# Optimization experiments

Measured on AMD Instinct MI355X. Metric: run time of the kernel, lower is better.

Reference implementation:

```python
import jax, jax.numpy as jnp
import numpy as np

B, L, D = 8192, 200, 64
NUM_ITEMS = 100000
HID = 64  # attention hidden_dim


def setup_inputs() -> dict:
    key = jax.random.key(0)
    ks = jax.random.split(key, 16)
    inp = {
        "item_sequence": jax.random.randint(ks[0], (B, L), 0, NUM_ITEMS),
        "click_sequence": jax.random.randint(ks[1], (B, L), 0, 2),
        "seq_length": jax.random.randint(ks[2], (B, 1), 1, L + 1),
        "target_item": jax.random.randint(ks[3], (B, 1), 0, NUM_ITEMS),
        "context_features": jax.random.normal(ks[4], (B, 9), dtype=jnp.float32),
        # embedding table (num_items+1, D)
        "emb_table": jax.random.normal(ks[5], (NUM_ITEMS + 1, D), dtype=jnp.float32) * 0.05,
        # attention MLP: Linear(2D->64), Linear(64->32), Linear(32->1)
        "aw1": jax.random.normal(ks[6], (2 * D, HID), dtype=jnp.float32) * 0.05,
        "ab1": jnp.zeros((HID,), jnp.float32),
        "aw2": jax.random.normal(ks[7], (HID, HID // 2), dtype=jnp.float32) * 0.05,
        "ab2": jnp.zeros((HID // 2,), jnp.float32),
        "aw3": jax.random.normal(ks[8], (HID // 2, 1), dtype=jnp.float32) * 0.05,
        "ab3": jnp.zeros((1,), jnp.float32),
        # context MLP: Linear(9->32)
        "cw": jax.random.normal(ks[9], (9, 32), dtype=jnp.float32) * 0.05,
        "cb": jnp.zeros((32,), jnp.float32),
        # head MLP: Linear(160->128), Linear(128->64), Linear(64->1)
        "mw1": jax.random.normal(ks[10], (2 * D + 32, 128), dtype=jnp.float32) * 0.05,
        "mb1": jnp.zeros((128,), jnp.float32),
        "mw2": jax.random.normal(ks[11], (128, 64), dtype=jnp.float32) * 0.05,
        "mb2": jnp.zeros((64,), jnp.float32),
        "mw3": jax.random.normal(ks[12], (64, 1), dtype=jnp.float32) * 0.05,
        "mb3": jnp.zeros((1,), jnp.float32),
    }
    return inp


def reference(item_sequence, click_sequence, seq_length, target_item, context_features,
              emb_table, aw1, ab1, aw2, ab2, aw3, ab3, cw, cb,
              mw1, mb1, mw2, mb2, mw3, mb3):
    seq_emb = emb_table[item_sequence]                 # [B, L, D]
    tgt_emb = emb_table[target_item[:, 0]]             # [B, D]
    seq_len = item_sequence.shape[1]
    mask = (jnp.arange(seq_len)[None, :] < seq_length).astype(seq_emb.dtype)  # [B, L]

    # DIN attention: concat(query, keys) -> 3-layer MLP -> masked softmax -> weighted sum
    q = jnp.broadcast_to(tgt_emb[:, None, :], seq_emb.shape)          # [B, L, D]
    att_in = jnp.concatenate([q, seq_emb], axis=-1)                   # [B, L, 2D]
    h = jax.nn.relu(att_in @ aw1 + ab1)
    h = jax.nn.relu(h @ aw2 + ab2)
    scores = (h @ aw3 + ab3)[..., 0]                                  # [B, L]
    scores = jnp.where(mask == 0, jnp.asarray(-1e9, scores.dtype), scores)
    w = jax.nn.softmax(scores, axis=1)                                # [B, L]
    attended = jnp.einsum('bl,bld->bd', w, seq_emb)                   # [B, D]

    ctx = jax.nn.relu(context_features @ cw + cb)                     # [B, 32]
    comb = jnp.concatenate([attended, tgt_emb, ctx], axis=1)          # [B, 2D+32]
    h = jax.nn.relu(comb @ mw1 + mb1)
    h = jax.nn.relu(h @ mw2 + mb2)
    out = jax.nn.sigmoid(h @ mw3 + mb3)[:, 0]                         # [B]
    return out
```

## Files before the change

kernel.cpp:

```cpp
#include <hip/hip_runtime.h>
#include <cmath>

typedef __attribute__((ext_vector_type(8))) short s16x8;
typedef __attribute__((ext_vector_type(4))) short s16x4;
typedef __attribute__((ext_vector_type(4))) float f32x4;

__device__ __forceinline__ short f2bf(float f) {
    union { float f; unsigned u; } v; v.f = f;
    unsigned r = v.u + 0x7FFFu + ((v.u >> 16) & 1u);
    return (short)(r >> 16);
}
__device__ __forceinline__ float bf2f(short s) {
    union { unsigned u; float f; } v; v.u = ((unsigned)(unsigned short)s) << 16;
    return v.f;
}

#define EMB_ELEMS 6400064
#define W1SEQ_SH  6400064
#define W1TOP_SH  6404160
#define W2_SH     6408256
#define MW1T_SH   6410304
#define MW2T_SH   6430784
#define QC_F      3219488
#define SC_F      3743776
#define CB_SH     10764352


__global__ __launch_bounds__(256)
void din_prep_kernel(const float* __restrict__ emb,
                     const float* __restrict__ aw1,
                     const float* __restrict__ aw2,
                     const float* __restrict__ mw1,
                     const float* __restrict__ mw2,
                     short* __restrict__ ws)
{
    const int bid = blockIdx.x;
    const int t = threadIdx.x;
    if (bid < 6251) {
        long e4 = ((long)bid * 256 + t) * 4;
        if (e4 < EMB_ELEMS) {
            float4 v = *(const float4*)(emb + e4);
            s16x4 bv = { f2bf(v.x), f2bf(v.y), f2bf(v.z), f2bf(v.w) };
            *(s16x4*)(ws + e4) = bv;
        }
        return;
    }
    const int wb = bid - 6251;
    if (wb == 0) {
        for (int idx = t; idx < 4096; idx += 256) {
            int j = idx & 7, lane = (idx >> 3) & 63, fr = idx >> 9;
            int n = (fr >> 1) * 16 + (lane & 15);
            int k = (fr & 1) * 32 + (lane >> 4) * 8 + j;
            ws[W1SEQ_SH + idx] = f2bf(aw1[(64 + k) * 64 + n]);
        }
    } else if (wb == 1) {
        for (int idx = t; idx < 4096; idx += 256) {
            int j = idx & 7, lane = (idx >> 3) & 63, fr = idx >> 9;
            int n = (fr >> 1) * 16 + (lane & 15);
            int k = (fr & 1) * 32 + (lane >> 4) * 8 + j;
            ws[W1TOP_SH + idx] = f2bf(aw1[k * 64 + n]);
        }
    } else if (wb == 2) {
        for (int idx = t; idx < 2048; idx += 256) {
            int j = idx & 7, lane = (idx >> 3) & 63, fr = idx >> 9;
            int n = (fr >> 1) * 16 + (lane & 15);
            int k = (fr & 1) * 32 + (lane >> 4) * 8 + j;
            ws[W2_SH + idx] = f2bf(aw2[k * 32 + n]);
        }
    } else if (wb == 3) {
        for (int idx = t; idx < 8192; idx += 256) {
            int j = idx & 7, lane = (idx >> 3) & 63, fr = idx >> 9;
            int n = (fr >> 2) * 16 + (lane & 15);
            int k = (fr & 3) * 32 + (lane >> 4) * 8 + j;
            ws[MW2T_SH + idx] = f2bf(mw2[k * 64 + n]);
        }
    } else {
        const int base = (wb - 4) * 5120;
        for (int ii = t; ii < 5120; ii += 256) {
            int idx = base + ii;
            int j = idx & 7, lane = (idx >> 3) & 63, fr = idx >> 9;
            int nt = fr / 5, ks = fr - nt * 5;
            int n = nt * 16 + (lane & 15);
            int k = ks * 32 + (lane >> 4) * 8 + j;
            ws[MW1T_SH + idx] = f2bf(mw1[k * 128 + n]);
        }
    }
}

__global__ __launch_bounds__(256)
void din_qc_kernel(const int* __restrict__ tgt_item,
                   const float* __restrict__ ab1,
                   short* __restrict__ ws)
{
    const int t = threadIdx.x, lane = t & 63, wave = t >> 6;
    const int quad = lane >> 4, r16 = lane & 15;
    const short* embbf = ws;
    const short* w1t   = ws + W1TOP_SH;
    float* qc = (float*)ws + QC_F;

    const int b0 = (blockIdx.x * 4 + wave) * 16;
    const int it = tgt_item[b0 + r16];
    const short* rp = embbf + it * 64 + quad * 8;
    s16x8 a0 = *(const s16x8*)(rp);
    s16x8 a1 = *(const s16x8*)(rp + 32);

    f32x4 acc[4] = {{0,0,0,0},{0,0,0,0},{0,0,0,0},{0,0,0,0}};
    #pragma unroll
    for (int nt = 0; nt < 4; ++nt) {
        s16x8 b_0 = *(const s16x8*)(w1t + ((nt * 2 + 0) * 64 + lane) * 8);
        s16x8 b_1 = *(const s16x8*)(w1t + ((nt * 2 + 1) * 64 + lane) * 8);
        acc[nt] = __builtin_amdgcn_mfma_f32_16x16x32_bf16(a0, b_0, acc[nt], 0, 0, 0);
        acc[nt] = __builtin_amdgcn_mfma_f32_16x16x32_bf16(a1, b_1, acc[nt], 0, 0, 0);
    }
    #pragma unroll
    for (int nt = 0; nt < 4; ++nt) {
        float bias = ab1[nt * 16 + r16];
        #pragma unroll
        for (int rr = 0; rr < 4; ++rr)
            qc[(b0 + quad * 4 + rr) * 64 + nt * 16 + r16] = acc[nt][rr] + bias;
    }
}

#define H1_PITCH 72
__global__ __launch_bounds__(256)
void din_att_kernel(const int* __restrict__ item_seq,
                    const int* __restrict__ seq_len_p,
                    const float* __restrict__ ab2,
                    const float* __restrict__ aw3, const float* __restrict__ ab3,
                    short* __restrict__ ws)
{
    const int t = threadIdx.x, lane = t & 63, wave = t >> 6;
    const int quad = lane >> 4, r16 = lane & 15;
    __shared__ short s_w1[4096];
    __shared__ short s_h1[4][16 * H1_PITCH];

    {
        const s16x8* src = (const s16x8*)(ws + W1SEQ_SH);
        s16x8* dst = (s16x8*)s_w1;
        for (int i = t; i < 512; i += 256) dst[i] = src[i];
    }
    __syncthreads();

    const int b    = blockIdx.x;
    const int len  = seq_len_p[b];
    const int row0 = wave * 64;
    if (row0 >= len) return;
    const int nc = min(4, (len - row0 + 15) >> 4);

    const short* embbf = ws;
    const float* qc    = (const float*)ws + QC_F + b * 64;
    float* scores      = (float*)ws + SC_F + b * 200;

    s16x8 af[4][2];
    #pragma unroll
    for (int ck = 0; ck < 4; ++ck) {
        if (ck < nc) {
            int r = row0 + ck * 16 + r16; if (r > 199) r = 199;
            const int it = item_seq[b * 200 + r];
            af[ck][0] = *(const s16x8*)(embbf + it * 64 + quad * 8);
            af[ck][1] = *(const s16x8*)(embbf + it * 64 + 32 + quad * 8);
        }
    }
    s16x8 w2r[4];
    #pragma unroll
    for (int fr = 0; fr < 4; ++fr)
        w2r[fr] = *(const s16x8*)(ws + W2_SH + (fr * 64 + lane) * 8);

    float qcv[4];
    #pragma unroll
    for (int nt = 0; nt < 4; ++nt) qcv[nt] = qc[nt * 16 + r16];
    const float bias2_lo = ab2[r16], bias2_hi = ab2[16 + r16];
    const float w3_lo    = aw3[r16], w3_hi    = aw3[16 + r16];
    const float b3       = ab3[0];
    short* h1w = s_h1[wave];

    #pragma unroll
    for (int ck = 0; ck < 4; ++ck) {
        if (ck >= nc) break;
        f32x4 acc[4] = {{0,0,0,0},{0,0,0,0},{0,0,0,0},{0,0,0,0}};
        #pragma unroll
        for (int nt = 0; nt < 4; ++nt) {
            s16x8 b_0 = *(const s16x8*)&s_w1[((nt * 2 + 0) * 64 + lane) * 8];
            s16x8 b_1 = *(const s16x8*)&s_w1[((nt * 2 + 1) * 64 + lane) * 8];
            acc[nt] = __builtin_amdgcn_mfma_f32_16x16x32_bf16(af[ck][0], b_0, acc[nt], 0, 0, 0);
            acc[nt] = __builtin_amdgcn_mfma_f32_16x16x32_bf16(af[ck][1], b_1, acc[nt], 0, 0, 0);
        }
        #pragma unroll
        for (int nt = 0; nt < 4; ++nt)
            #pragma unroll
            for (int rr = 0; rr < 4; ++rr) {
                float v = fmaxf(acc[nt][rr] + qcv[nt], 0.f);
                h1w[(quad * 4 + rr) * H1_PITCH + nt * 16 + r16] = f2bf(v);
            }
        __builtin_amdgcn_wave_barrier();

        s16x8 h0  = *(const s16x8*)&h1w[r16 * H1_PITCH + quad * 8];
        s16x8 h1v = *(const s16x8*)&h1w[r16 * H1_PITCH + 32 + quad * 8];
        f32x4 c2[2] = {{0,0,0,0},{0,0,0,0}};
        #pragma unroll
        for (int nt = 0; nt < 2; ++nt) {
            c2[nt] = __builtin_amdgcn_mfma_f32_16x16x32_bf16(h0,  w2r[nt * 2],     c2[nt], 0, 0, 0);
            c2[nt] = __builtin_amdgcn_mfma_f32_16x16x32_bf16(h1v, w2r[nt * 2 + 1], c2[nt], 0, 0, 0);
        }
        #pragma unroll
        for (int rr = 0; rr < 4; ++rr) {
            float p = fmaxf(c2[0][rr] + bias2_lo, 0.f) * w3_lo
                    + fmaxf(c2[1][rr] + bias2_hi, 0.f) * w3_hi;
            p += __shfl_xor(p, 8);
            p += __shfl_xor(p, 4);
            p += __shfl_xor(p, 2);
            p += __shfl_xor(p, 1);
            int orow = row0 + ck * 16 + quad * 4 + rr;
            if (r16 == 0 && orow < 200) scores[orow] = p + b3;
        }
        __builtin_amdgcn_wave_barrier();
    }
}

__global__ __launch_bounds__(256)
void din_pool_kernel(const int* __restrict__ item_seq,
                     const int* __restrict__ seq_len_p,
                     const int* __restrict__ tgt_item,
                     const float* __restrict__ ctx_feat,
                     const float* __restrict__ cw,  const float* __restrict__ cb,
                     short* __restrict__ ws)
{
    const int t = threadIdx.x, lane = t & 63, wave = t >> 6;
    const int quad = lane >> 4, r16 = lane & 15;
    __shared__ float s_w[4][200];

    const int b   = blockIdx.x * 4 + wave;
    const int len = seq_len_p[b];
    const short* embbf = ws;
    const float* sc    = (const float*)ws + SC_F + b * 200;
    short* comb        = ws + CB_SH + b * 160;

    float m = -1e30f;
    for (int l = lane; l < len; l += 64) m = fmaxf(m, sc[l]);
    #pragma unroll
    for (int off = 32; off; off >>= 1) m = fmaxf(m, __shfl_xor(m, off));
    float e = 0.f;
    for (int l = lane; l < len; l += 64) {
        float v = __expf(sc[l] - m);
        s_w[wave][l] = v;
        e += v;
    }
    #pragma unroll
    for (int off = 32; off; off >>= 1) e += __shfl_xor(e, off);
    const float inv = 1.f / e;
    __builtin_amdgcn_wave_barrier();

    float a0 = 0.f, a1 = 0.f, a2 = 0.f, a3 = 0.f;
    for (int l = quad; l < len; l += 8) {
        const int it0 = item_seq[b * 200 + l];
        s16x4 v0 = *(const s16x4*)(embbf + it0 * 64 + r16 * 4);
        const int l1 = l + 4;
        const bool live1 = l1 < len;
        s16x4 v1 = {};
        if (live1) {
            const int it1 = item_seq[b * 200 + l1];
            v1 = *(const s16x4*)(embbf + it1 * 64 + r16 * 4);
        }
        const float w0 = s_w[wave][l];
        const float w1 = live1 ? s_w[wave][l1] : 0.f;
        a0 += w0 * bf2f(v0.x) + w1 * bf2f(v1.x);
        a1 += w0 * bf2f(v0.y) + w1 * bf2f(v1.y);
        a2 += w0 * bf2f(v0.z) + w1 * bf2f(v1.z);
        a3 += w0 * bf2f(v0.w) + w1 * bf2f(v1.w);
    }
    a0 += __shfl_xor(a0, 16); a0 += __shfl_xor(a0, 32);
    a1 += __shfl_xor(a1, 16); a1 += __shfl_xor(a1, 32);
    a2 += __shfl_xor(a2, 16); a2 += __shfl_xor(a2, 32);
    a3 += __shfl_xor(a3, 16); a3 += __shfl_xor(a3, 32);
    if (quad == 0) {
        s16x4 bv = { f2bf(a0 * inv), f2bf(a1 * inv), f2bf(a2 * inv), f2bf(a3 * inv) };
        *(s16x4*)(comb + r16 * 4) = bv;
    }
    comb[64 + lane] = embbf[tgt_item[b] * 64 + lane];
    if (lane < 32) {
        float a = cb[lane];
        #pragma unroll
        for (int k = 0; k < 9; ++k) a += ctx_feat[b * 9 + k] * cw[k * 32 + lane];
        comb[128 + lane] = f2bf(fmaxf(a, 0.f));
    }
}

__global__ __launch_bounds__(256)
void din_mlp_kernel(const float* __restrict__ mb1,
                    const float* __restrict__ mb2,
                    const float* __restrict__ mw3, const float* __restrict__ mb3,
                    const short* __restrict__ ws,
                    float* __restrict__ out)
{
    const int t = threadIdx.x, lane = t & 63, wave = t >> 6;
    const int quad = lane >> 4, r16 = lane & 15;
    __shared__ short s_h1[4][16 * 136];
    __shared__ short s_h2[4][16 * 72];

    const int b0 = (blockIdx.x * 4 + wave) * 16;
    const short* comb = ws + CB_SH;
    const short* w1   = ws + MW1T_SH;
    const short* w2   = ws + MW2T_SH;

    s16x8 a[5];
    #pragma unroll
    for (int ks = 0; ks < 5; ++ks)
        a[ks] = *(const s16x8*)(comb + (b0 + r16) * 160 + ks * 32 + quad * 8);
    f32x4 acc[8] = {{0,0,0,0},{0,0,0,0},{0,0,0,0},{0,0,0,0},{0,0,0,0},{0,0,0,0},{0,0,0,0},{0,0,0,0}};
    #pragma unroll
    for (int nt = 0; nt < 8; ++nt)
        #pragma unroll
        for (int ks = 0; ks < 5; ++ks) {
            s16x8 bf = *(const s16x8*)(w1 + ((nt * 5 + ks) * 64 + lane) * 8);
            acc[nt] = __builtin_amdgcn_mfma_f32_16x16x32_bf16(a[ks], bf, acc[nt], 0, 0, 0);
        }
    #pragma unroll
    for (int nt = 0; nt < 8; ++nt) {
        float bias = mb1[nt * 16 + r16];
        #pragma unroll
        for (int rr = 0; rr < 4; ++rr)
            s_h1[wave][(quad * 4 + rr) * 136 + nt * 16 + r16] = f2bf(fmaxf(acc[nt][rr] + bias, 0.f));
    }
    __builtin_amdgcn_wave_barrier();

    s16x8 a2[4];
    #pragma unroll
    for (int ks = 0; ks < 4; ++ks)
        a2[ks] = *(const s16x8*)&s_h1[wave][r16 * 136 + ks * 32 + quad * 8];
    f32x4 acc2[4] = {{0,0,0,0},{0,0,0,0},{0,0,0,0},{0,0,0,0}};
    #pragma unroll
    for (int nt = 0; nt < 4; ++nt)
        #pragma unroll
        for (int ks = 0; ks < 4; ++ks) {
            s16x8 bf = *(const s16x8*)(w2 + ((nt * 4 + ks) * 64 + lane) * 8);
            acc2[nt] = __builtin_amdgcn_mfma_f32_16x16x32_bf16(a2[ks], bf, acc2[nt], 0, 0, 0);
        }
    #pragma unroll
    for (int nt = 0; nt < 4; ++nt) {
        float bias = mb2[nt * 16 + r16];
        #pragma unroll
        for (int rr = 0; rr < 4; ++rr)
            s_h2[wave][(quad * 4 + rr) * 72 + nt * 16 + r16] = f2bf(fmaxf(acc2[nt][rr] + bias, 0.f));
    }
    __builtin_amdgcn_wave_barrier();

    float p = 0.f;
    #pragma unroll
    for (int j = 0; j < 16; ++j)
        p += bf2f(s_h2[wave][r16 * 72 + quad * 16 + j]) * mw3[quad * 16 + j];
    p += __shfl_xor(p, 16);
    p += __shfl_xor(p, 32);
    if (quad == 0) out[b0 + r16] = 1.f / (1.f + __expf(-(p + mb3[0])));
}

extern "C" void kernel_launch(void* const* d_in, const int* in_sizes, int n_in,
                              void* d_out, int out_size, void* d_ws, size_t ws_size,
                              hipStream_t stream)
{
    const int*   item_seq  = (const int*)  d_in[0];
    const int*   seq_len   = (const int*)  d_in[2];
    const int*   tgt_item  = (const int*)  d_in[3];
    const float* ctx_feat  = (const float*)d_in[4];
    const float* emb       = (const float*)d_in[5];
    const float* aw1 = (const float*)d_in[6];
    const float* ab1 = (const float*)d_in[7];
    const float* aw2 = (const float*)d_in[8];
    const float* ab2 = (const float*)d_in[9];
    const float* aw3 = (const float*)d_in[10];
    const float* ab3 = (const float*)d_in[11];
    const float* cw  = (const float*)d_in[12];
    const float* cb  = (const float*)d_in[13];
    const float* mw1 = (const float*)d_in[14];
    const float* mb1 = (const float*)d_in[15];
    const float* mw2 = (const float*)d_in[16];
    const float* mb2 = (const float*)d_in[17];
    const float* mw3 = (const float*)d_in[18];
    const float* mb3 = (const float*)d_in[19];
    float* out = (float*)d_out;
    short* ws  = (short*)d_ws;

    hipLaunchKernelGGL(din_prep_kernel, dim3(6259), dim3(256), 0, stream,
                       emb, aw1, aw2, mw1, mw2, ws);
    hipLaunchKernelGGL(din_qc_kernel, dim3(128), dim3(256), 0, stream,
                       tgt_item, ab1, ws);
    hipLaunchKernelGGL(din_att_kernel, dim3(8192), dim3(256), 0, stream,
                       item_seq, seq_len, ab2, aw3, ab3, ws);
    hipLaunchKernelGGL(din_pool_kernel, dim3(2048), dim3(256), 0, stream,
                       item_seq, seq_len, tgt_item, ctx_feat, cw, cb, ws);
    hipLaunchKernelGGL(din_mlp_kernel, dim3(128), dim3(256), 0, stream,
                       mb1, mb2, mw3, mb3, ws, out);
}
```

Before: 197.8 us.

## Fuse query projection, attention scoring, softmax and pooling into one per-batch kernel

Folds the target-query projection, attention MLP scoring, masked softmax, weighted pooling and the context MLP into a single kernel with one block per batch row. Scores stay in shared memory, and the pooling reuses the embedding fragments already held in registers instead of gathering them from global memory a second time. This removes two kernel launches, the global round trip for scores and qc, and the duplicate embedding gather. The head MLP kernel is also reshaped into one wave per block with more blocks. In exchange, every block now does a mostly wasted MFMA for the single query row and pays extra block-wide syncs.

```diff
diff --git a/kernel.cpp b/kernel.cpp
--- a/kernel.cpp
+++ b/kernel.cpp
@@ -21,10 +21,7 @@
 #define W2_SH     6408256
 #define MW1T_SH   6410304
 #define MW2T_SH   6430784
-#define QC_F      3219488
-#define SC_F      3743776
 #define CB_SH     10764352
-
 
 __global__ __launch_bounds__(256)
 void din_prep_kernel(const float* __restrict__ emb,
@@ -87,70 +84,42 @@
     }
 }
 
-__global__ __launch_bounds__(256)
-void din_qc_kernel(const int* __restrict__ tgt_item,
-                   const float* __restrict__ ab1,
-                   short* __restrict__ ws)
-{
-    const int t = threadIdx.x, lane = t & 63, wave = t >> 6;
-    const int quad = lane >> 4, r16 = lane & 15;
-    const short* embbf = ws;
-    const short* w1t   = ws + W1TOP_SH;
-    float* qc = (float*)ws + QC_F;
-
-    const int b0 = (blockIdx.x * 4 + wave) * 16;
-    const int it = tgt_item[b0 + r16];
-    const short* rp = embbf + it * 64 + quad * 8;
-    s16x8 a0 = *(const s16x8*)(rp);
-    s16x8 a1 = *(const s16x8*)(rp + 32);
-
-    f32x4 acc[4] = {{0,0,0,0},{0,0,0,0},{0,0,0,0},{0,0,0,0}};
-    #pragma unroll
-    for (int nt = 0; nt < 4; ++nt) {
-        s16x8 b_0 = *(const s16x8*)(w1t + ((nt * 2 + 0) * 64 + lane) * 8);
-        s16x8 b_1 = *(const s16x8*)(w1t + ((nt * 2 + 1) * 64 + lane) * 8);
-        acc[nt] = __builtin_amdgcn_mfma_f32_16x16x32_bf16(a0, b_0, acc[nt], 0, 0, 0);
-        acc[nt] = __builtin_amdgcn_mfma_f32_16x16x32_bf16(a1, b_1, acc[nt], 0, 0, 0);
-    }
-    #pragma unroll
-    for (int nt = 0; nt < 4; ++nt) {
-        float bias = ab1[nt * 16 + r16];
-        #pragma unroll
-        for (int rr = 0; rr < 4; ++rr)
-            qc[(b0 + quad * 4 + rr) * 64 + nt * 16 + r16] = acc[nt][rr] + bias;
-    }
-}
-
 #define H1_PITCH 72
 __global__ __launch_bounds__(256)
-void din_att_kernel(const int* __restrict__ item_seq,
-                    const int* __restrict__ seq_len_p,
-                    const float* __restrict__ ab2,
-                    const float* __restrict__ aw3, const float* __restrict__ ab3,
-                    short* __restrict__ ws)
+void din_att_fused(const int* __restrict__ item_seq,
+                   const int* __restrict__ seq_len_p,
+                   const int* __restrict__ tgt_item,
+                   const float* __restrict__ ctx_feat,
+                   const float* __restrict__ ab1,
+                   const float* __restrict__ ab2,
+                   const float* __restrict__ aw3, const float* __restrict__ ab3,
+                   const float* __restrict__ cw,  const float* __restrict__ cb,
+                   short* __restrict__ ws)
 {
     const int t = threadIdx.x, lane = t & 63, wave = t >> 6;
     const int quad = lane >> 4, r16 = lane & 15;
     __shared__ short s_w1[4096];
     __shared__ short s_h1[4][16 * H1_PITCH];
+    __shared__ float s_sc[208];
+    __shared__ float s_qc[64];
+    __shared__ float s_pool[4][64];
+    __shared__ float s_ctx[32];
+    __shared__ float s_inv;
+
+    const int b   = blockIdx.x;
+    const int len = seq_len_p[b];
+    const int tgt = tgt_item[b];
+    const short* embbf = ws;
 
     {
         const s16x8* src = (const s16x8*)(ws + W1SEQ_SH);
         s16x8* dst = (s16x8*)s_w1;
-        for (int i = t; i < 512; i += 256) dst[i] = src[i];
-    }
-    __syncthreads();
-
-    const int b    = blockIdx.x;
-    const int len  = seq_len_p[b];
+        dst[t]       = src[t];
+        dst[t + 256] = src[t + 256];
+    }
+
     const int row0 = wave * 64;
-    if (row0 >= len) return;
-    const int nc = min(4, (len - row0 + 15) >> 4);
-
-    const short* embbf = ws;
-    const float* qc    = (const float*)ws + QC_F + b * 64;
-    float* scores      = (float*)ws + SC_F + b * 200;
-
+    const int nc = (row0 < len) ? min(4, (len - row0 + 15) >> 4) : 0;
     s16x8 af[4][2];
     #pragma unroll
     for (int ck = 0; ck < 4; ++ck) {
@@ -165,13 +134,35 @@
     #pragma unroll
     for (int fr = 0; fr < 4; ++fr)
         w2r[fr] = *(const s16x8*)(ws + W2_SH + (fr * 64 + lane) * 8);
-
-    float qcv[4];
-    #pragma unroll
-    for (int nt = 0; nt < 4; ++nt) qcv[nt] = qc[nt * 16 + r16];
     const float bias2_lo = ab2[r16], bias2_hi = ab2[16 + r16];
     const float w3_lo    = aw3[r16], w3_hi    = aw3[16 + r16];
     const float b3       = ab3[0];
+
+    if (wave == 0) {
+        s16x8 a0 = {}, a1 = {};
+        if (r16 == 0) {
+            a0 = *(const s16x8*)(embbf + tgt * 64 + quad * 8);
+            a1 = *(const s16x8*)(embbf + tgt * 64 + 32 + quad * 8);
+        }
+        f32x4 qacc[4] = {{0,0,0,0},{0,0,0,0},{0,0,0,0},{0,0,0,0}};
+        #pragma unroll
+        for (int nt = 0; nt < 4; ++nt) {
+            s16x8 b_0 = *(const s16x8*)(ws + W1TOP_SH + ((nt * 2 + 0) * 64 + lane) * 8);
+            s16x8 b_1 = *(const s16x8*)(ws + W1TOP_SH + ((nt * 2 + 1) * 64 + lane) * 8);
+            qacc[nt] = __builtin_amdgcn_mfma_f32_16x16x32_bf16(a0, b_0, qacc[nt], 0, 0, 0);
+            qacc[nt] = __builtin_amdgcn_mfma_f32_16x16x32_bf16(a1, b_1, qacc[nt], 0, 0, 0);
+        }
+        if (quad == 0) {
+            #pragma unroll
+            for (int nt = 0; nt < 4; ++nt)
+                s_qc[nt * 16 + r16] = qacc[nt][0] + ab1[nt * 16 + r16];
+        }
+    }
+    __syncthreads();
+
+    float qcv[4];
+    #pragma unroll
+    for (int nt = 0; nt < 4; ++nt) qcv[nt] = s_qc[nt * 16 + r16];
     short* h1w = s_h1[wave];
 
     #pragma unroll
@@ -211,93 +202,90 @@
             p += __shfl_xor(p, 2);
             p += __shfl_xor(p, 1);
             int orow = row0 + ck * 16 + quad * 4 + rr;
-            if (r16 == 0 && orow < 200) scores[orow] = p + b3;
+            if (r16 == 0 && orow < 200) s_sc[orow] = p + b3;
         }
         __builtin_amdgcn_wave_barrier();
     }
-}
-
-__global__ __launch_bounds__(256)
-void din_pool_kernel(const int* __restrict__ item_seq,
-                     const int* __restrict__ seq_len_p,
-                     const int* __restrict__ tgt_item,
-                     const float* __restrict__ ctx_feat,
-                     const float* __restrict__ cw,  const float* __restrict__ cb,
-                     short* __restrict__ ws)
-{
-    const int t = threadIdx.x, lane = t & 63, wave = t >> 6;
-    const int quad = lane >> 4, r16 = lane & 15;
-    __shared__ float s_w[4][200];
-
-    const int b   = blockIdx.x * 4 + wave;
-    const int len = seq_len_p[b];
-    const short* embbf = ws;
-    const float* sc    = (const float*)ws + SC_F + b * 200;
-    short* comb        = ws + CB_SH + b * 160;
-
-    float m = -1e30f;
-    for (int l = lane; l < len; l += 64) m = fmaxf(m, sc[l]);
-    #pragma unroll
-    for (int off = 32; off; off >>= 1) m = fmaxf(m, __shfl_xor(m, off));
-    float e = 0.f;
-    for (int l = lane; l < len; l += 64) {
-        float v = __expf(sc[l] - m);
-        s_w[wave][l] = v;
-        e += v;
-    }
-    #pragma unroll
-    for (int off = 32; off; off >>= 1) e += __shfl_xor(e, off);
-    const float inv = 1.f / e;
-    __builtin_amdgcn_wave_barrier();
-
-    float a0 = 0.f, a1 = 0.f, a2 = 0.f, a3 = 0.f;
-    for (int l = quad; l < len; l += 8) {
-        const int it0 = item_seq[b * 200 + l];
-        s16x4 v0 = *(const s16x4*)(embbf + it0 * 64 + r16 * 4);
-        const int l1 = l + 4;
-        const bool live1 = l1 < len;
-        s16x4 v1 = {};
-        if (live1) {
-            const int it1 = item_seq[b * 200 + l1];
-            v1 = *(const s16x4*)(embbf + it1 * 64 + r16 * 4);
-        }
-        const float w0 = s_w[wave][l];
-        const float w1 = live1 ? s_w[wave][l1] : 0.f;
-        a0 += w0 * bf2f(v0.x) + w1 * bf2f(v1.x);
-        a1 += w0 * bf2f(v0.y) + w1 * bf2f(v1.y);
-        a2 += w0 * bf2f(v0.z) + w1 * bf2f(v1.z);
-        a3 += w0 * bf2f(v0.w) + w1 * bf2f(v1.w);
-    }
-    a0 += __shfl_xor(a0, 16); a0 += __shfl_xor(a0, 32);
-    a1 += __shfl_xor(a1, 16); a1 += __shfl_xor(a1, 32);
-    a2 += __shfl_xor(a2, 16); a2 += __shfl_xor(a2, 32);
-    a3 += __shfl_xor(a3, 16); a3 += __shfl_xor(a3, 32);
-    if (quad == 0) {
-        s16x4 bv = { f2bf(a0 * inv), f2bf(a1 * inv), f2bf(a2 * inv), f2bf(a3 * inv) };
-        *(s16x4*)(comb + r16 * 4) = bv;
-    }
-    comb[64 + lane] = embbf[tgt_item[b] * 64 + lane];
-    if (lane < 32) {
-        float a = cb[lane];
-        #pragma unroll
-        for (int k = 0; k < 9; ++k) a += ctx_feat[b * 9 + k] * cw[k * 32 + lane];
-        comb[128 + lane] = f2bf(fmaxf(a, 0.f));
-    }
-}
-
-__global__ __launch_bounds__(256)
+    __syncthreads();
+
+    short* comb = ws + CB_SH + b * 160;
+    if (wave == 0) {
+        float m = -1e30f;
+        for (int l = lane; l < len; l += 64) m = fmaxf(m, s_sc[l]);
+        #pragma unroll
+        for (int off = 32; off; off >>= 1) m = fmaxf(m, __shfl_xor(m, off));
+        float e = 0.f;
+        for (int l = lane; l < len; l += 64) {
+            float v = __expf(s_sc[l] - m);
+            s_sc[l] = v;
+            e += v;
+        }
+        #pragma unroll
+        for (int off = 32; off; off >>= 1) e += __shfl_xor(e, off);
+        if (lane == 0) s_inv = 1.f / e;
+    } else if (wave == 1) {
+        if (lane < 32) {
+            float a = cb[lane];
+            #pragma unroll
+            for (int k = 0; k < 9; ++k) a += ctx_feat[b * 9 + k] * cw[k * 32 + lane];
+            s_ctx[lane] = fmaxf(a, 0.f);
+        }
+    } else if (wave == 2) {
+        comb[64 + lane] = embbf[tgt * 64 + lane];
+    }
+    __syncthreads();
+
+    float p[16];
+    #pragma unroll
+    for (int i = 0; i < 16; ++i) p[i] = 0.f;
+    #pragma unroll
+    for (int ck = 0; ck < 4; ++ck) {
+        if (ck >= nc) break;
+        const int row = row0 + ck * 16 + r16;
+        const float w = (row < len) ? s_sc[row] : 0.f;
+        #pragma unroll
+        for (int j = 0; j < 8; ++j) {
+            p[j]     += w * bf2f(af[ck][0][j]);
+            p[8 + j] += w * bf2f(af[ck][1][j]);
+        }
+    }
+    #pragma unroll
+    for (int i = 0; i < 16; ++i) {
+        p[i] += __shfl_xor(p[i], 1);
+        p[i] += __shfl_xor(p[i], 2);
+        p[i] += __shfl_xor(p[i], 4);
+        p[i] += __shfl_xor(p[i], 8);
+    }
+    if (r16 == 0) {
+        #pragma unroll
+        for (int j = 0; j < 8; ++j) {
+            s_pool[wave][quad * 8 + j]      = p[j];
+            s_pool[wave][32 + quad * 8 + j] = p[8 + j];
+        }
+    }
+    __syncthreads();
+
+    if (t < 64) {
+        float a = (s_pool[0][t] + s_pool[1][t] + s_pool[2][t] + s_pool[3][t]) * s_inv;
+        comb[t] = f2bf(a);
+    } else if (t < 96) {
+        comb[128 + (t - 64)] = f2bf(s_ctx[t - 64]);
+    }
+}
+
+__global__ __launch_bounds__(64)
 void din_mlp_kernel(const float* __restrict__ mb1,
                     const float* __restrict__ mb2,
                     const float* __restrict__ mw3, const float* __restrict__ mb3,
                     const short* __restrict__ ws,
                     float* __restrict__ out)
 {
-    const int t = threadIdx.x, lane = t & 63, wave = t >> 6;
+    const int lane = threadIdx.x & 63;
     const int quad = lane >> 4, r16 = lane & 15;
-    __shared__ short s_h1[4][16 * 136];
-    __shared__ short s_h2[4][16 * 72];
-
-    const int b0 = (blockIdx.x * 4 + wave) * 16;
+    __shared__ short s_h1[16 * 136];
+    __shared__ short s_h2[16 * 72];
+
+    const int b0 = blockIdx.x * 16;
     const short* comb = ws + CB_SH;
     const short* w1   = ws + MW1T_SH;
     const short* w2   = ws + MW2T_SH;
@@ -319,14 +307,14 @@
         float bias = mb1[nt * 16 + r16];
         #pragma unroll
         for (int rr = 0; rr < 4; ++rr)
-            s_h1[wave][(quad * 4 + rr) * 136 + nt * 16 + r16] = f2bf(fmaxf(acc[nt][rr] + bias, 0.f));
+            s_h1[(quad * 4 + rr) * 136 + nt * 16 + r16] = f2bf(fmaxf(acc[nt][rr] + bias, 0.f));
     }
     __builtin_amdgcn_wave_barrier();
 
     s16x8 a2[4];
     #pragma unroll
     for (int ks = 0; ks < 4; ++ks)
-        a2[ks] = *(const s16x8*)&s_h1[wave][r16 * 136 + ks * 32 + quad * 8];
+        a2[ks] = *(const s16x8*)&s_h1[r16 * 136 + ks * 32 + quad * 8];
     f32x4 acc2[4] = {{0,0,0,0},{0,0,0,0},{0,0,0,0},{0,0,0,0}};
     #pragma unroll
     for (int nt = 0; nt < 4; ++nt)
@@ -340,14 +328,14 @@
         float bias = mb2[nt * 16 + r16];
         #pragma unroll
         for (int rr = 0; rr < 4; ++rr)
-            s_h2[wave][(quad * 4 + rr) * 72 + nt * 16 + r16] = f2bf(fmaxf(acc2[nt][rr] + bias, 0.f));
+            s_h2[(quad * 4 + rr) * 72 + nt * 16 + r16] = f2bf(fmaxf(acc2[nt][rr] + bias, 0.f));
     }
     __builtin_amdgcn_wave_barrier();
 
     float p = 0.f;
     #pragma unroll
     for (int j = 0; j < 16; ++j)
-        p += bf2f(s_h2[wave][r16 * 72 + quad * 16 + j]) * mw3[quad * 16 + j];
+        p += bf2f(s_h2[r16 * 72 + quad * 16 + j]) * mw3[quad * 16 + j];
     p += __shfl_xor(p, 16);
     p += __shfl_xor(p, 32);
     if (quad == 0) out[b0 + r16] = 1.f / (1.f + __expf(-(p + mb3[0])));
@@ -381,12 +369,9 @@
 
     hipLaunchKernelGGL(din_prep_kernel, dim3(6259), dim3(256), 0, stream,
                        emb, aw1, aw2, mw1, mw2, ws);
-    hipLaunchKernelGGL(din_qc_kernel, dim3(128), dim3(256), 0, stream,
-                       tgt_item, ab1, ws);
-    hipLaunchKernelGGL(din_att_kernel, dim3(8192), dim3(256), 0, stream,
-                       item_seq, seq_len, ab2, aw3, ab3, ws);
-    hipLaunchKernelGGL(din_pool_kernel, dim3(2048), dim3(256), 0, stream,
-                       item_seq, seq_len, tgt_item, ctx_feat, cw, cb, ws);
-    hipLaunchKernelGGL(din_mlp_kernel, dim3(128), dim3(256), 0, stream,
+    hipLaunchKernelGGL(din_att_fused, dim3(8192), dim3(256), 0, stream,
+                       item_seq, seq_len, tgt_item, ctx_feat,
+                       ab1, ab2, aw3, ab3, cw, cb, ws);
+    hipLaunchKernelGGL(din_mlp_kernel, dim3(512), dim3(64), 0, stream,
                        mb1, mb2, mw3, mb3, ws, out);
 }
```

Measured after the change: 213.2 us. +7.8%, slower.
